# Optimization experiments

Measured on AMD Instinct MI355X. Metric: run time of the kernel, lower is better.

Reference implementation:

```python
import jax, jax.numpy as jnp
import numpy as np

B, S, D = 1024, 64, 768      # batch, patch_num, embed_dim
POOL, TOPK = 30, 4           # prompt pool size, top-k
SEQ = TOPK + S               # 68 = args.prompt_length + patch_num
CT = 64                      # compress_token
LN_EPS = 1e-5


def _l2_normalize(x, axis):
    ss = jnp.sum(x * x, axis=axis, keepdims=True)
    return x * jax.lax.rsqrt(jnp.maximum(ss, 1e-12))


def _layernorm(x, g, b):
    m = jnp.mean(x, axis=-1, keepdims=True)
    v = jnp.mean((x - m) ** 2, axis=-1, keepdims=True)
    return (x - m) * jax.lax.rsqrt(v + LN_EPS) * g + b


def setup_inputs() -> dict:
    key = jax.random.key(0)
    ks = jax.random.split(key, 8)
    def lin(k, din, dout):
        return (jax.random.normal(k, (din, dout), jnp.float32) / np.sqrt(din)).astype(jnp.float32)
    return {
        "x_embed": jax.random.normal(ks[0], (B, S, D), jnp.float32),
        "prompt": jax.random.uniform(ks[1], (POOL, D), jnp.float32, -5.0, 5.0),
        # mlp_1: Linear(SEQ->CT), LN(CT), Linear(CT->CT), LN(CT)
        "w1a": lin(ks[2], SEQ, CT), "b1a": jnp.zeros((CT,), jnp.float32),
        "g1a": jnp.ones((CT,), jnp.float32), "be1a": jnp.zeros((CT,), jnp.float32),
        "w1b": lin(ks[3], CT, CT), "b1b": jnp.zeros((CT,), jnp.float32),
        "g1b": jnp.ones((CT,), jnp.float32), "be1b": jnp.zeros((CT,), jnp.float32),
        # mlp_2: Linear(D->D), LN(D), Linear(D->D), LN(D)
        "w2a": lin(ks[4], D, D), "b2a": jnp.zeros((D,), jnp.float32),
        "g2a": jnp.ones((D,), jnp.float32), "be2a": jnp.zeros((D,), jnp.float32),
        "w2b": lin(ks[5], D, D), "b2b": jnp.zeros((D,), jnp.float32),
        "g2b": jnp.ones((D,), jnp.float32), "be2b": jnp.zeros((D,), jnp.float32),
    }


def _mixer(x, w1a, b1a, g1a, be1a, w1b, b1b, g1b, be1b,
           w2a, b2a, g2a, be2a, w2b, b2b, g2b, be2b):
    # x: (B, SEQ, D)
    x = jnp.swapaxes(x, 1, 2)                                   # (B, D, SEQ)
    x = _layernorm(jax.nn.relu(x @ w1a + b1a), g1a, be1a)       # (B, D, CT)
    x = _layernorm(jax.nn.relu(x @ w1b + b1b), g1b, be1b)
    x = jnp.swapaxes(x, 1, 2)                                   # (B, CT, D)
    x = _layernorm(jax.nn.relu(x @ w2a + b2a), g2a, be2a)
    x = _layernorm(jax.nn.relu(x @ w2b + b2b), g2b, be2b)
    return x


def reference(x_embed, prompt,
              w1a, b1a, g1a, be1a, w1b, b1b, g1b, be1b,
              w2a, b2a, g2a, be2a, w2b, b2b, g2b, be2b):
    # embedding key: mean over sequence
    x_mean = jnp.mean(x_embed, axis=1)                  # (B, D)
    prompt_norm = _l2_normalize(prompt, axis=1)         # (POOL, D)
    x_norm = _l2_normalize(x_mean, axis=1)              # (B, D)
    similarity = x_norm @ prompt_norm.T                 # (B, POOL)
    _, idx = jax.lax.top_k(similarity, TOPK)            # (B, TOPK), sorted desc
    batched_prompt = prompt[idx]                        # (B, TOPK, D)  (length=1 collapsed)
    selected_key = prompt_norm[idx]                     # (B, TOPK, D)
    reduce_sim = jnp.sum(selected_key * x_norm[:, None, :]) / x_embed.shape[0]
    x = jnp.concatenate([batched_prompt, x_embed], axis=1)  # (B, SEQ, D)
    prompted = _mixer(x, w1a, b1a, g1a, be1a, w1b, b1b, g1b, be1b,
                      w2a, b2a, g2a, be2a, w2b, b2b, g2b, be2b)  # (B, CT, D)
    return prompted, reduce_sim, similarity, idx
```

## Files before the change

### kernel.cpp

```cpp
#include <hip/hip_runtime.h>

#define B_    1024
#define S_    64
#define D_    768
#define POOL_ 30
#define TOPK_ 4
#define SEQ_  68
#define CT_   64

#define OUT_NP    50331648ull
#define OUT_RSIM  50331648ull
#define OUT_SIM   50331649ull
#define OUT_IDX   50362369ull

typedef short s16x8 __attribute__((ext_vector_type(8)));
typedef float f32x4 __attribute__((ext_vector_type(4)));
typedef unsigned short u16;

__device__ __forceinline__ u16 f2bf(float f){
  unsigned u = __float_as_uint(f);
  u += 0x7fff + ((u >> 16) & 1);
  return (u16)(u >> 16);
}

__global__ void prep_small(const float* __restrict__ prompt,
                           const float* __restrict__ w1a,
                           const float* __restrict__ w1b,
                           float* __restrict__ pnorm2,
                           u16* __restrict__ w1aT, u16* __restrict__ w1bT){
  int t = threadIdx.x;
  if (blockIdx.x == 0){
    if (t < 240){
      int j = t >> 3, seg = t & 7;
      float s = 0.f;
      for (int d = seg*96; d < seg*96 + 96; ++d){ float v = prompt[j*768 + d]; s += v*v; }
      #pragma unroll
      for (int m = 1; m < 8; m <<= 1) s += __shfl_xor(s, m);
      if (seg == 0) pnorm2[j] = rsqrtf(fmaxf(s, 1e-12f));
    }
  } else if (blockIdx.x == 1){
    for (int e = t; e < 6144; e += 256){
      int frag = e >> 3, el = e & 7;
      int lane = frag & 63, tile = frag >> 6;
      int nt = tile / 3, ks = tile % 3;
      int k  = ks*32 + (lane >> 4)*8 + el;
      int ct = nt*16 + (lane & 15);
      w1aT[e] = f2bf(k < SEQ_ ? w1a[k*64 + ct] : 0.f);
    }
  } else {
    for (int e = t; e < 4096; e += 256){
      int frag = e >> 3, el = e & 7;
      int lane = frag & 63, tile = frag >> 6;
      int nt = tile >> 1, ks = tile & 1;
      int k  = ks*32 + (lane >> 4)*8 + el;
      int n  = nt*16 + (lane & 15);
      w1bT[e] = f2bf(w1b[k*64 + n]);
    }
  }
}

__global__ void pack_w(const float* __restrict__ w2a,
                       const float* __restrict__ w2b,
                       u16* __restrict__ Wpka, u16* __restrict__ Wpkb){
  int lane = threadIdx.x;
  int ntg = blockIdx.x, ks = blockIdx.y;
  const float* w = blockIdx.z ? w2b : w2a;
  u16* wp = (blockIdx.z ? Wpkb : Wpka) + ((size_t)(ntg*24 + ks)*64 + lane)*8;
  int n  = ntg*16 + (lane & 15);
  int k0 = ks*32 + (lane >> 4)*8;
  #pragma unroll
  for (int e = 0; e < 8; ++e) wp[e] = f2bf(w[(size_t)(k0 + e)*768 + n]);
}

__global__ void sim_topk(const float* __restrict__ xe,
                         const float* __restrict__ prompt,
                         const float* __restrict__ pnorm2,
                         float* __restrict__ out, int* __restrict__ idx_int){
  __shared__ f32x4 ps[4][192];
  __shared__ f32x4 xm4s[192];
  __shared__ float wred[4];
  __shared__ float rsx_sh;
  __shared__ float simv[30];
  int b = blockIdx.x, t = threadIdx.x;
  int lane = t & 63, wv = t >> 6;

  const f32x4* xrow = (const f32x4*)(xe + (size_t)b*64*768);
  f32x4 a0 = {0.f,0.f,0.f,0.f}, a1 = a0, a2 = a0;
  #pragma unroll
  for (int r = 0; r < 16; ++r){
    const f32x4* rp = xrow + (size_t)(wv*16 + r)*192;
    a0 += rp[lane]; a1 += rp[lane + 64]; a2 += rp[lane + 128];
  }
  ps[wv][lane] = a0; ps[wv][lane + 64] = a1; ps[wv][lane + 128] = a2;
  __syncthreads();

  if (t < 192){
    f32x4 s = ps[0][t] + ps[1][t] + ps[2][t] + ps[3][t];
    s *= (1.f/64.f);
    xm4s[t] = s;
  }
  __syncthreads();

  if (wv == 0){
    f32x4 v0 = xm4s[lane], v1 = xm4s[lane + 64], v2 = xm4s[lane + 128];
    float n = v0[0]*v0[0]+v0[1]*v0[1]+v0[2]*v0[2]+v0[3]*v0[3]
            + v1[0]*v1[0]+v1[1]*v1[1]+v1[2]*v1[2]+v1[3]*v1[3]
            + v2[0]*v2[0]+v2[1]*v2[1]+v2[2]*v2[2]+v2[3]*v2[3];
    #pragma unroll
    for (int m = 1; m < 64; m <<= 1) n += __shfl_xor(n, m);
    if (lane == 0) rsx_sh = rsqrtf(fmaxf(n, 1e-12f));
  }
  __syncthreads();

  if (t < 240){
    int j = t >> 3, seg = t & 7;
    const f32x4* pj = (const f32x4*)(prompt + j*768) + seg*24;
    const f32x4* xm = xm4s + seg*24;
    float s = 0.f;
    #pragma unroll
    for (int i = 0; i < 24; ++i){
      f32x4 p = pj[i], x = xm[i];
      s += p[0]*x[0] + p[1]*x[1] + p[2]*x[2] + p[3]*x[3];
    }
    #pragma unroll
    for (int m = 1; m < 8; m <<= 1) s += __shfl_xor(s, m);
    if (seg == 0){
      float sim = s * rsx_sh * pnorm2[j];
      out[OUT_SIM + (size_t)b*30 + j] = sim;
      simv[j] = sim;
    }
  }
  __syncthreads();

  if (t == 0){
    float racc = 0.f;
    for (int k = 0; k < 4; ++k){
      float best = -1e30f; int bi = 0;
      for (int j = 0; j < 30; ++j){ float v = simv[j]; if (v > best){ best = v; bi = j; } }
      simv[bi] = -1e30f;
      idx_int[b*4 + k] = bi;
      out[OUT_IDX + (size_t)b*4 + k] = (float)bi;
      racc += best;
    }
    atomicAdd(&out[OUT_RSIM], racc * (1.f/1024.f));
  }
}

__global__ void stage1(const float* __restrict__ xe, const float* __restrict__ prompt,
                       const int* __restrict__ idx_int,
                       const u16* __restrict__ w1aT, const u16* __restrict__ w1bT,
                       const float* __restrict__ b1a, const float* __restrict__ g1a, const float* __restrict__ be1a,
                       const float* __restrict__ b1b, const float* __restrict__ g1b, const float* __restrict__ be1b,
                       u16* __restrict__ Tg){
  __shared__ __align__(16) unsigned char sm[43136];
  u16* As_pk      = (u16*)sm;
  u16 (*A2s)[72]  = (u16(*)[72])(sm + 24704);
  u16 (*Ts)[136]  = (u16(*)[136])sm;

  int t = threadIdx.x;
  int b = blockIdx.y, d0 = blockIdx.x * 128;

  #pragma unroll
  for (int p = 0; p < 12; ++p){
    int item = t + 512*p;
    int dd = item & 127, jp = item >> 7;
    int j = jp << 1;
    float v0 = 0.f, v1 = 0.f;
    if (j < 4){
      v0 = prompt[(size_t)idx_int[b*4 + j    ]*768 + d0 + dd];
      v1 = prompt[(size_t)idx_int[b*4 + j + 1]*768 + d0 + dd];
    } else if (j < 68){
      const float* xp = xe + ((size_t)b*64 + (j-4))*768 + d0 + dd;
      v0 = xp[0];
      v1 = xp[768];
    }
    unsigned pk = (unsigned)f2bf(v0) | ((unsigned)f2bf(v1) << 16);
    int idx16 = (dd>>4)*1544 + (j>>5)*512 + ((j>>3)&3)*128 + (dd&15)*8 + (j&7);
    *(unsigned*)&As_pk[idx16] = pk;
  }
  __syncthreads();

  int wv = t >> 6, lane = t & 63, quad = lane >> 4, l15 = lane & 15;
  int mrow = wv*16 + l15;

  f32x4 acc[4];
  #pragma unroll
  for (int nt = 0; nt < 4; ++nt) acc[nt] = (f32x4){0.f,0.f,0.f,0.f};
  #pragma unroll
  for (int ks = 0; ks < 3; ++ks){
    s16x8 a = *(const s16x8*)&As_pk[wv*1544 + ks*512 + lane*8];
    #pragma unroll
    for (int nt = 0; nt < 4; ++nt){
      s16x8 bf = *(const s16x8*)(w1aT + ((nt*3 + ks)*64 + lane)*8);
      acc[nt] = __builtin_amdgcn_mfma_f32_16x16x32_bf16(a, bf, acc[nt], 0, 0, 0);
    }
  }
  {
    float s1[4] = {0,0,0,0}, s2[4] = {0,0,0,0};
    #pragma unroll
    for (int nt = 0; nt < 4; ++nt){
      float bb = b1a[nt*16 + l15];
      #pragma unroll
      for (int i = 0; i < 4; ++i){
        float v = fmaxf(acc[nt][i] + bb, 0.f);
        acc[nt][i] = v; s1[i] += v; s2[i] += v*v;
      }
    }
    #pragma unroll
    for (int i = 0; i < 4; ++i){
      #pragma unroll
      for (int m = 1; m < 16; m <<= 1){ s1[i] += __shfl_xor(s1[i], m); s2[i] += __shfl_xor(s2[i], m); }
    }
    #pragma unroll
    for (int i = 0; i < 4; ++i){
      float mean = s1[i]*(1.f/64.f);
      float var  = s2[i]*(1.f/64.f) - mean*mean;
      float rs   = rsqrtf(var + 1e-5f);
      int row = wv*16 + quad*4 + i;
      #pragma unroll
      for (int nt = 0; nt < 4; ++nt){
        int ct = nt*16 + l15;
        A2s[row][ct] = f2bf((acc[nt][i] - mean)*rs*g1a[ct] + be1a[ct]);
      }
    }
  }
  __syncthreads();

  f32x4 acc2[4];
  #pragma unroll
  for (int nt = 0; nt < 4; ++nt) acc2[nt] = (f32x4){0.f,0.f,0.f,0.f};
  #pragma unroll
  for (int ks = 0; ks < 2; ++ks){
    s16x8 a = *(const s16x8*)&A2s[mrow][ks*32 + quad*8];
    #pragma unroll
    for (int nt = 0; nt < 4; ++nt){
      s16x8 bf = *(const s16x8*)(w1bT + ((nt*2 + ks)*64 + lane)*8);
      acc2[nt] = __builtin_amdgcn_mfma_f32_16x16x32_bf16(a, bf, acc2[nt], 0, 0, 0);
    }
  }
  {
    float s1[4] = {0,0,0,0}, s2[4] = {0,0,0,0};
    #pragma unroll
    for (int nt = 0; nt < 4; ++nt){
      float bb = b1b[nt*16 + l15];
      #pragma unroll
      for (int i = 0; i < 4; ++i){
        float v = fmaxf(acc2[nt][i] + bb, 0.f);
        acc2[nt][i] = v; s1[i] += v; s2[i] += v*v;
      }
    }
    #pragma unroll
    for (int i = 0; i < 4; ++i){
      #pragma unroll
      for (int m = 1; m < 16; m <<= 1){ s1[i] += __shfl_xor(s1[i], m); s2[i] += __shfl_xor(s2[i], m); }
    }
    #pragma unroll
    for (int i = 0; i < 4; ++i){
      float mean = s1[i]*(1.f/64.f);
      float var  = s2[i]*(1.f/64.f) - mean*mean;
      float rs   = rsqrtf(var + 1e-5f);
      int row = wv*16 + quad*4 + i;
      #pragma unroll
      for (int nt = 0; nt < 4; ++nt){
        int ct = nt*16 + l15;
        Ts[ct][row] = f2bf((acc2[nt][i] - mean)*rs*g1b[ct] + be1b[ct]);
      }
    }
  }
  __syncthreads();

  #pragma unroll
  for (int c = t; c < 1024; c += 512){
    int ct = c >> 4, off = (c & 15)*8;
    *(s16x8*)(Tg + ((size_t)(b*64 + ct))*768 + d0 + off) = *(const s16x8*)&Ts[ct][off];
  }
}

__device__ __forceinline__ void gemm_ln_768(
    const u16* __restrict__ Wpk, const float* __restrict__ bias,
    const float* __restrict__ g, const float* __restrict__ be,
    u16 (*Arows)[776], float (*red)[64][8], float (*redt)[64],
    float* __restrict__ outp, int row0, int t, bool final_store)
{
  int wv = t >> 6, lane = t & 63, quad = lane >> 4, l15 = lane & 15;
  f32x4 acc[4][6];
  #pragma unroll
  for (int mt = 0; mt < 4; ++mt)
    #pragma unroll
    for (int nt = 0; nt < 6; ++nt) acc[mt][nt] = (f32x4){0.f,0.f,0.f,0.f};

  const u16* wbase = Wpk + (size_t)wv*73728 + (size_t)lane*8;

  s16x8 bnxt[6];
  #pragma unroll
  for (int nt = 0; nt < 6; ++nt)
    bnxt[nt] = *(const s16x8*)(wbase + nt*12288);

  #pragma unroll
  for (int ks = 0; ks < 24; ++ks){
    s16x8 bcur[6];
    #pragma unroll
    for (int nt = 0; nt < 6; ++nt) bcur[nt] = bnxt[nt];
    if (ks < 23){
      #pragma unroll
      for (int nt = 0; nt < 6; ++nt)
        bnxt[nt] = *(const s16x8*)(wbase + nt*12288 + (ks+1)*512);
    }
    s16x8 a[4];
    #pragma unroll
    for (int mt = 0; mt < 4; ++mt)
      a[mt] = *(const s16x8*)&Arows[mt*16 + l15][ks*32 + quad*8];
    #pragma unroll
    for (int nt = 0; nt < 6; ++nt){
      #pragma unroll
      for (int mt = 0; mt < 4; ++mt)
        acc[mt][nt] = __builtin_amdgcn_mfma_f32_16x16x32_bf16(a[mt], bcur[nt], acc[mt][nt], 0, 0, 0);
    }
  }

  float s1[4][4], s2[4][4];
  #pragma unroll
  for (int mt = 0; mt < 4; ++mt)
    #pragma unroll
    for (int i = 0; i < 4; ++i){ s1[mt][i] = 0.f; s2[mt][i] = 0.f; }
  #pragma unroll
  for (int nt = 0; nt < 6; ++nt){
    float bb = bias[wv*96 + nt*16 + l15];
    #pragma unroll
    for (int mt = 0; mt < 4; ++mt){
      #pragma unroll
      for (int i = 0; i < 4; ++i){
        float v = fmaxf(acc[mt][nt][i] + bb, 0.f);
        acc[mt][nt][i] = v; s1[mt][i] += v; s2[mt][i] += v*v;
      }
    }
  }
  #pragma unroll
  for (int mt = 0; mt < 4; ++mt){
    #pragma unroll
    for (int i = 0; i < 4; ++i){
      #pragma unroll
      for (int m = 1; m < 16; m <<= 1){
        s1[mt][i] += __shfl_xor(s1[mt][i], m);
        s2[mt][i] += __shfl_xor(s2[mt][i], m);
      }
    }
  }
  if (l15 == 0){
    #pragma unroll
    for (int mt = 0; mt < 4; ++mt)
      #pragma unroll
      for (int i = 0; i < 4; ++i){
        int row = mt*16 + quad*4 + i;
        red[0][row][wv] = s1[mt][i]; red[1][row][wv] = s2[mt][i];
      }
  }
  __syncthreads();
  if (t < 128){
    int r = t >> 1, p = t & 1;
    float s = 0.f;
    #pragma unroll
    for (int w = 0; w < 8; ++w) s += red[p][r][w];
    redt[p][r] = s;
  }
  __syncthreads();
  #pragma unroll
  for (int mt = 0; mt < 4; ++mt){
    #pragma unroll
    for (int i = 0; i < 4; ++i){
      int row = mt*16 + quad*4 + i;
      float mean = redt[0][row]*(1.f/768.f);
      float var  = redt[1][row]*(1.f/768.f) - mean*mean;
      float rs   = rsqrtf(var + 1e-5f);
      #pragma unroll
      for (int nt = 0; nt < 6; ++nt){
        int col = wv*96 + nt*16 + l15;
        float v = (acc[mt][nt][i] - mean)*rs*g[col] + be[col];
        if (final_store) outp[(size_t)(row0 + row)*768 + col] = v;
        else             Arows[row][col] = f2bf(v);
      }
    }
  }
}

__global__ __launch_bounds__(512, 2)
void stage2(const u16* __restrict__ Tg,
            const u16* __restrict__ Wpka, const u16* __restrict__ Wpkb,
            const float* __restrict__ b2a, const float* __restrict__ g2a, const float* __restrict__ be2a,
            const float* __restrict__ b2b, const float* __restrict__ g2b, const float* __restrict__ be2b,
            float* __restrict__ out){
  __shared__ __align__(16) u16 Arows[64][776];
  __shared__ float red[2][64][8];
  __shared__ float redt[2][64];
  int t = threadIdx.x;
  int row0 = blockIdx.x * 64;
  #pragma unroll
  for (int c = t; c < 6144; c += 512){
    int r = c / 96, off = (c % 96)*8;
    *(s16x8*)&Arows[r][off] = *(const s16x8*)(Tg + (size_t)(row0 + r)*768 + off);
  }
  __syncthreads();
  gemm_ln_768(Wpka, b2a, g2a, be2a, Arows, red, redt, out, row0, t, false);
  __syncthreads();
  gemm_ln_768(Wpkb, b2b, g2b, be2b, Arows, red, redt, out, row0, t, true);
}

extern "C" void kernel_launch(void* const* d_in, const int* in_sizes, int n_in,
                              void* d_out, int out_size, void* d_ws, size_t ws_size,
                              hipStream_t stream){
  (void)in_sizes; (void)n_in; (void)out_size; (void)ws_size;
  const float* xe     = (const float*)d_in[0];
  const float* prompt = (const float*)d_in[1];
  const float* w1a = (const float*)d_in[2],  *b1a = (const float*)d_in[3];
  const float* g1a = (const float*)d_in[4],  *be1a= (const float*)d_in[5];
  const float* w1b = (const float*)d_in[6],  *b1b = (const float*)d_in[7];
  const float* g1b = (const float*)d_in[8],  *be1b= (const float*)d_in[9];
  const float* w2a = (const float*)d_in[10], *b2a = (const float*)d_in[11];
  const float* g2a = (const float*)d_in[12], *be2a= (const float*)d_in[13];
  const float* w2b = (const float*)d_in[14], *b2b = (const float*)d_in[15];
  const float* g2b = (const float*)d_in[16], *be2b= (const float*)d_in[17];
  float* out = (float*)d_out;

  char* ws = (char*)d_ws;
  u16*   Tg     = (u16*)(ws);
  u16*   Wpka   = (u16*)(ws + 100663296);
  u16*   Wpkb   = (u16*)(ws + 101842944);
  u16*   w1aT   = (u16*)(ws + 103022592);
  u16*   w1bT   = (u16*)(ws + 103034880);
  float* pnorm2 = (float*)(ws + 103043072);
  int*   idx_i  = (int*)(ws + 103043200);

  hipMemsetAsync((char*)d_out + OUT_RSIM*sizeof(float), 0, sizeof(float), stream);
  prep_small<<<3, 256, 0, stream>>>(prompt, w1a, w1b, pnorm2, w1aT, w1bT);
  pack_w<<<dim3(48,24,2), 64, 0, stream>>>(w2a, w2b, Wpka, Wpkb);
  sim_topk<<<B_, 256, 0, stream>>>(xe, prompt, pnorm2, out, idx_i);
  stage1<<<dim3(6, B_), 512, 0, stream>>>(xe, prompt, idx_i, w1aT, w1bT,
                                          b1a, g1a, be1a, b1b, g1b, be1b, Tg);
  stage2<<<1024, 512, 0, stream>>>(Tg, Wpka, Wpkb, b2a, g2a, be2a, b2b, g2b, be2b, out);
}
```

Before: 637.5 us.

## Fuse sim/topk, token-mixing and channel MLP into one per-batch kernel

```diff
diff --git a/kernel.cpp b/kernel.cpp
--- a/kernel.cpp
+++ b/kernel.cpp
@@ -21,6 +21,10 @@
   unsigned u = __float_as_uint(f);
   u += 0x7fff + ((u >> 16) & 1);
   return (u16)(u >> 16);
+}
+
+__device__ __forceinline__ int ar_idx(int row, int col){
+  return row*776 + (col & ~63) + ((((col >> 3) + row) & 7) << 3) + (col & 7);
 }
 
 __global__ void prep_small(const float* __restrict__ prompt,
@@ -72,217 +76,15 @@
   for (int e = 0; e < 8; ++e) wp[e] = f2bf(w[(size_t)(k0 + e)*768 + n]);
 }
 
-__global__ void sim_topk(const float* __restrict__ xe,
-                         const float* __restrict__ prompt,
-                         const float* __restrict__ pnorm2,
-                         float* __restrict__ out, int* __restrict__ idx_int){
-  __shared__ f32x4 ps[4][192];
-  __shared__ f32x4 xm4s[192];
-  __shared__ float wred[4];
-  __shared__ float rsx_sh;
-  __shared__ float simv[30];
-  int b = blockIdx.x, t = threadIdx.x;
-  int lane = t & 63, wv = t >> 6;
-
-  const f32x4* xrow = (const f32x4*)(xe + (size_t)b*64*768);
-  f32x4 a0 = {0.f,0.f,0.f,0.f}, a1 = a0, a2 = a0;
-  #pragma unroll
-  for (int r = 0; r < 16; ++r){
-    const f32x4* rp = xrow + (size_t)(wv*16 + r)*192;
-    a0 += rp[lane]; a1 += rp[lane + 64]; a2 += rp[lane + 128];
-  }
-  ps[wv][lane] = a0; ps[wv][lane + 64] = a1; ps[wv][lane + 128] = a2;
-  __syncthreads();
-
-  if (t < 192){
-    f32x4 s = ps[0][t] + ps[1][t] + ps[2][t] + ps[3][t];
-    s *= (1.f/64.f);
-    xm4s[t] = s;
-  }
-  __syncthreads();
-
-  if (wv == 0){
-    f32x4 v0 = xm4s[lane], v1 = xm4s[lane + 64], v2 = xm4s[lane + 128];
-    float n = v0[0]*v0[0]+v0[1]*v0[1]+v0[2]*v0[2]+v0[3]*v0[3]
-            + v1[0]*v1[0]+v1[1]*v1[1]+v1[2]*v1[2]+v1[3]*v1[3]
-            + v2[0]*v2[0]+v2[1]*v2[1]+v2[2]*v2[2]+v2[3]*v2[3];
-    #pragma unroll
-    for (int m = 1; m < 64; m <<= 1) n += __shfl_xor(n, m);
-    if (lane == 0) rsx_sh = rsqrtf(fmaxf(n, 1e-12f));
-  }
-  __syncthreads();
-
-  if (t < 240){
-    int j = t >> 3, seg = t & 7;
-    const f32x4* pj = (const f32x4*)(prompt + j*768) + seg*24;
-    const f32x4* xm = xm4s + seg*24;
-    float s = 0.f;
-    #pragma unroll
-    for (int i = 0; i < 24; ++i){
-      f32x4 p = pj[i], x = xm[i];
-      s += p[0]*x[0] + p[1]*x[1] + p[2]*x[2] + p[3]*x[3];
-    }
-    #pragma unroll
-    for (int m = 1; m < 8; m <<= 1) s += __shfl_xor(s, m);
-    if (seg == 0){
-      float sim = s * rsx_sh * pnorm2[j];
-      out[OUT_SIM + (size_t)b*30 + j] = sim;
-      simv[j] = sim;
-    }
-  }
-  __syncthreads();
-
-  if (t == 0){
-    float racc = 0.f;
-    for (int k = 0; k < 4; ++k){
-      float best = -1e30f; int bi = 0;
-      for (int j = 0; j < 30; ++j){ float v = simv[j]; if (v > best){ best = v; bi = j; } }
-      simv[bi] = -1e30f;
-      idx_int[b*4 + k] = bi;
-      out[OUT_IDX + (size_t)b*4 + k] = (float)bi;
-      racc += best;
-    }
-    atomicAdd(&out[OUT_RSIM], racc * (1.f/1024.f));
-  }
-}
-
-__global__ void stage1(const float* __restrict__ xe, const float* __restrict__ prompt,
-                       const int* __restrict__ idx_int,
-                       const u16* __restrict__ w1aT, const u16* __restrict__ w1bT,
-                       const float* __restrict__ b1a, const float* __restrict__ g1a, const float* __restrict__ be1a,
-                       const float* __restrict__ b1b, const float* __restrict__ g1b, const float* __restrict__ be1b,
-                       u16* __restrict__ Tg){
-  __shared__ __align__(16) unsigned char sm[43136];
-  u16* As_pk      = (u16*)sm;
-  u16 (*A2s)[72]  = (u16(*)[72])(sm + 24704);
-  u16 (*Ts)[136]  = (u16(*)[136])sm;
-
-  int t = threadIdx.x;
-  int b = blockIdx.y, d0 = blockIdx.x * 128;
-
-  #pragma unroll
-  for (int p = 0; p < 12; ++p){
-    int item = t + 512*p;
-    int dd = item & 127, jp = item >> 7;
-    int j = jp << 1;
-    float v0 = 0.f, v1 = 0.f;
-    if (j < 4){
-      v0 = prompt[(size_t)idx_int[b*4 + j    ]*768 + d0 + dd];
-      v1 = prompt[(size_t)idx_int[b*4 + j + 1]*768 + d0 + dd];
-    } else if (j < 68){
-      const float* xp = xe + ((size_t)b*64 + (j-4))*768 + d0 + dd;
-      v0 = xp[0];
-      v1 = xp[768];
-    }
-    unsigned pk = (unsigned)f2bf(v0) | ((unsigned)f2bf(v1) << 16);
-    int idx16 = (dd>>4)*1544 + (j>>5)*512 + ((j>>3)&3)*128 + (dd&15)*8 + (j&7);
-    *(unsigned*)&As_pk[idx16] = pk;
-  }
-  __syncthreads();
-
-  int wv = t >> 6, lane = t & 63, quad = lane >> 4, l15 = lane & 15;
-  int mrow = wv*16 + l15;
-
-  f32x4 acc[4];
-  #pragma unroll
-  for (int nt = 0; nt < 4; ++nt) acc[nt] = (f32x4){0.f,0.f,0.f,0.f};
-  #pragma unroll
-  for (int ks = 0; ks < 3; ++ks){
-    s16x8 a = *(const s16x8*)&As_pk[wv*1544 + ks*512 + lane*8];
-    #pragma unroll
-    for (int nt = 0; nt < 4; ++nt){
-      s16x8 bf = *(const s16x8*)(w1aT + ((nt*3 + ks)*64 + lane)*8);
-      acc[nt] = __builtin_amdgcn_mfma_f32_16x16x32_bf16(a, bf, acc[nt], 0, 0, 0);
-    }
-  }
-  {
-    float s1[4] = {0,0,0,0}, s2[4] = {0,0,0,0};
-    #pragma unroll
-    for (int nt = 0; nt < 4; ++nt){
-      float bb = b1a[nt*16 + l15];
-      #pragma unroll
-      for (int i = 0; i < 4; ++i){
-        float v = fmaxf(acc[nt][i] + bb, 0.f);
-        acc[nt][i] = v; s1[i] += v; s2[i] += v*v;
-      }
-    }
-    #pragma unroll
-    for (int i = 0; i < 4; ++i){
-      #pragma unroll
-      for (int m = 1; m < 16; m <<= 1){ s1[i] += __shfl_xor(s1[i], m); s2[i] += __shfl_xor(s2[i], m); }
-    }
-    #pragma unroll
-    for (int i = 0; i < 4; ++i){
-      float mean = s1[i]*(1.f/64.f);
-      float var  = s2[i]*(1.f/64.f) - mean*mean;
-      float rs   = rsqrtf(var + 1e-5f);
-      int row = wv*16 + quad*4 + i;
-      #pragma unroll
-      for (int nt = 0; nt < 4; ++nt){
-        int ct = nt*16 + l15;
-        A2s[row][ct] = f2bf((acc[nt][i] - mean)*rs*g1a[ct] + be1a[ct]);
-      }
-    }
-  }
-  __syncthreads();
-
-  f32x4 acc2[4];
-  #pragma unroll
-  for (int nt = 0; nt < 4; ++nt) acc2[nt] = (f32x4){0.f,0.f,0.f,0.f};
-  #pragma unroll
-  for (int ks = 0; ks < 2; ++ks){
-    s16x8 a = *(const s16x8*)&A2s[mrow][ks*32 + quad*8];
-    #pragma unroll
-    for (int nt = 0; nt < 4; ++nt){
-      s16x8 bf = *(const s16x8*)(w1bT + ((nt*2 + ks)*64 + lane)*8);
-      acc2[nt] = __builtin_amdgcn_mfma_f32_16x16x32_bf16(a, bf, acc2[nt], 0, 0, 0);
-    }
-  }
-  {
-    float s1[4] = {0,0,0,0}, s2[4] = {0,0,0,0};
-    #pragma unroll
-    for (int nt = 0; nt < 4; ++nt){
-      float bb = b1b[nt*16 + l15];
-      #pragma unroll
-      for (int i = 0; i < 4; ++i){
-        float v = fmaxf(acc2[nt][i] + bb, 0.f);
-        acc2[nt][i] = v; s1[i] += v; s2[i] += v*v;
-      }
-    }
-    #pragma unroll
-    for (int i = 0; i < 4; ++i){
-      #pragma unroll
-      for (int m = 1; m < 16; m <<= 1){ s1[i] += __shfl_xor(s1[i], m); s2[i] += __shfl_xor(s2[i], m); }
-    }
-    #pragma unroll
-    for (int i = 0; i < 4; ++i){
-      float mean = s1[i]*(1.f/64.f);
-      float var  = s2[i]*(1.f/64.f) - mean*mean;
-      float rs   = rsqrtf(var + 1e-5f);
-      int row = wv*16 + quad*4 + i;
-      #pragma unroll
-      for (int nt = 0; nt < 4; ++nt){
-        int ct = nt*16 + l15;
-        Ts[ct][row] = f2bf((acc2[nt][i] - mean)*rs*g1b[ct] + be1b[ct]);
-      }
-    }
-  }
-  __syncthreads();
-
-  #pragma unroll
-  for (int c = t; c < 1024; c += 512){
-    int ct = c >> 4, off = (c & 15)*8;
-    *(s16x8*)(Tg + ((size_t)(b*64 + ct))*768 + d0 + off) = *(const s16x8*)&Ts[ct][off];
-  }
-}
-
+template<bool FINAL>
 __device__ __forceinline__ void gemm_ln_768(
     const u16* __restrict__ Wpk, const float* __restrict__ bias,
     const float* __restrict__ g, const float* __restrict__ be,
-    u16 (*Arows)[776], float (*red)[64][8], float (*redt)[64],
-    float* __restrict__ outp, int row0, int t, bool final_store)
+    u16* __restrict__ Arows, float (*red)[64][8], float (*redt)[64],
+    float* __restrict__ outp, int row0, int t)
 {
   int wv = t >> 6, lane = t & 63, quad = lane >> 4, l15 = lane & 15;
+  int h = l15 & 7;
   f32x4 acc[4][6];
   #pragma unroll
   for (int mt = 0; mt < 4; ++mt)
@@ -291,32 +93,46 @@
 
   const u16* wbase = Wpk + (size_t)wv*73728 + (size_t)lane*8;
 
-  s16x8 bnxt[6];
-  #pragma unroll
-  for (int nt = 0; nt < 6; ++nt)
-    bnxt[nt] = *(const s16x8*)(wbase + nt*12288);
-
-  #pragma unroll
-  for (int ks = 0; ks < 24; ++ks){
-    s16x8 bcur[6];
-    #pragma unroll
-    for (int nt = 0; nt < 6; ++nt) bcur[nt] = bnxt[nt];
-    if (ks < 23){
-      #pragma unroll
-      for (int nt = 0; nt < 6; ++nt)
-        bnxt[nt] = *(const s16x8*)(wbase + nt*12288 + (ks+1)*512);
-    }
-    s16x8 a[4];
-    #pragma unroll
-    for (int mt = 0; mt < 4; ++mt)
-      a[mt] = *(const s16x8*)&Arows[mt*16 + l15][ks*32 + quad*8];
-    #pragma unroll
-    for (int nt = 0; nt < 6; ++nt){
-      #pragma unroll
-      for (int mt = 0; mt < 4; ++mt)
-        acc[mt][nt] = __builtin_amdgcn_mfma_f32_16x16x32_bf16(a[mt], bcur[nt], acc[mt][nt], 0, 0, 0);
-    }
-  }
+  const u16* Ap0[4]; const u16* Ap1[4];
+  #pragma unroll
+  for (int mt = 0; mt < 4; ++mt){
+    int rb = (mt*16 + l15)*776;
+    Ap0[mt] = Arows + rb + (((quad     + h) & 7) << 3);
+    Ap1[mt] = Arows + rb + (((quad + 4 + h) & 7) << 3);
+  }
+
+  s16x8 bX[6], bY[6], bZ[6];
+  #pragma unroll
+  for (int nt = 0; nt < 6; ++nt) bX[nt] = *(const s16x8*)(wbase + nt*12288);
+  #pragma unroll
+  for (int nt = 0; nt < 6; ++nt) bY[nt] = *(const s16x8*)(wbase + nt*12288 + 512);
+
+#define GSTEP(CUR, PRE, KS)                                                    \
+  {                                                                            \
+    if ((KS)+2 < 24){                                                          \
+      _Pragma("unroll")                                                        \
+      for (int nt = 0; nt < 6; ++nt)                                           \
+        PRE[nt] = *(const s16x8*)(wbase + nt*12288 + ((KS)+2)*512);            \
+    }                                                                          \
+    s16x8 a_[4];                                                               \
+    _Pragma("unroll")                                                          \
+    for (int mt = 0; mt < 4; ++mt)                                             \
+      a_[mt] = *(const s16x8*)(( ((KS)&1) ? Ap1[mt] : Ap0[mt] ) + ((KS)>>1)*64);\
+    _Pragma("unroll")                                                          \
+    for (int nt = 0; nt < 6; ++nt){                                            \
+      _Pragma("unroll")                                                        \
+      for (int mt = 0; mt < 4; ++mt)                                           \
+        acc[mt][nt] = __builtin_amdgcn_mfma_f32_16x16x32_bf16(a_[mt], CUR[nt], acc[mt][nt], 0, 0, 0); \
+    }                                                                          \
+  }
+
+  #pragma unroll
+  for (int kp = 0; kp < 8; ++kp){
+    GSTEP(bX, bZ, kp*3+0)
+    GSTEP(bY, bX, kp*3+1)
+    GSTEP(bZ, bY, kp*3+2)
+  }
+#undef GSTEP
 
   float s1[4][4], s2[4][4];
   #pragma unroll
@@ -376,33 +192,219 @@
       for (int nt = 0; nt < 6; ++nt){
         int col = wv*96 + nt*16 + l15;
         float v = (acc[mt][nt][i] - mean)*rs*g[col] + be[col];
-        if (final_store) outp[(size_t)(row0 + row)*768 + col] = v;
-        else             Arows[row][col] = f2bf(v);
+        if (FINAL) outp[(size_t)(row0 + row)*768 + col] = v;
+        else       Arows[ar_idx(row, col)] = f2bf(v);
       }
     }
   }
 }
 
 __global__ __launch_bounds__(512, 2)
-void stage2(const u16* __restrict__ Tg,
-            const u16* __restrict__ Wpka, const u16* __restrict__ Wpkb,
-            const float* __restrict__ b2a, const float* __restrict__ g2a, const float* __restrict__ be2a,
-            const float* __restrict__ b2b, const float* __restrict__ g2b, const float* __restrict__ be2b,
-            float* __restrict__ out){
-  __shared__ __align__(16) u16 Arows[64][776];
+void fused(const float* __restrict__ xe, const float* __restrict__ prompt,
+           const float* __restrict__ pnorm2,
+           const u16* __restrict__ w1aT, const u16* __restrict__ w1bT,
+           const float* __restrict__ b1a, const float* __restrict__ g1a, const float* __restrict__ be1a,
+           const float* __restrict__ b1b, const float* __restrict__ g1b, const float* __restrict__ be1b,
+           const u16* __restrict__ Wpka, const u16* __restrict__ Wpkb,
+           const float* __restrict__ b2a, const float* __restrict__ g2a, const float* __restrict__ be2a,
+           const float* __restrict__ b2b, const float* __restrict__ g2b, const float* __restrict__ be2b,
+           float* __restrict__ out)
+{
+  __shared__ __align__(16) u16 Arows[64*776];
+  __shared__ __align__(16) unsigned char scr[43136];
   __shared__ float red[2][64][8];
   __shared__ float redt[2][64];
-  int t = threadIdx.x;
-  int row0 = blockIdx.x * 64;
-  #pragma unroll
-  for (int c = t; c < 6144; c += 512){
-    int r = c / 96, off = (c % 96)*8;
-    *(s16x8*)&Arows[r][off] = *(const s16x8*)(Tg + (size_t)(row0 + r)*768 + off);
-  }
+  __shared__ float simv[30];
+  __shared__ float rsx_sh;
+  __shared__ int   idxs[4];
+
+  int b = blockIdx.x, t = threadIdx.x;
+  int lane = t & 63, wv = t >> 6, quad = lane >> 4, l15 = lane & 15;
+
+  {
+    f32x4 (*ps)[192] = (f32x4(*)[192])scr;
+    f32x4* xm4s = (f32x4*)(scr + 24576);
+    const f32x4* xrow = (const f32x4*)(xe + (size_t)b*49152);
+    f32x4 a0 = {0.f,0.f,0.f,0.f}, a1 = a0, a2 = a0;
+    #pragma unroll
+    for (int r = 0; r < 8; ++r){
+      const f32x4* rp = xrow + (size_t)(wv*8 + r)*192;
+      a0 += rp[lane]; a1 += rp[lane + 64]; a2 += rp[lane + 128];
+    }
+    ps[wv][lane] = a0; ps[wv][lane + 64] = a1; ps[wv][lane + 128] = a2;
+    __syncthreads();
+    if (t < 192){
+      f32x4 s = ps[0][t];
+      #pragma unroll
+      for (int w = 1; w < 8; ++w) s += ps[w][t];
+      s *= (1.f/64.f);
+      xm4s[t] = s;
+    }
+    __syncthreads();
+    if (wv == 0){
+      f32x4 v0 = xm4s[lane], v1 = xm4s[lane + 64], v2 = xm4s[lane + 128];
+      float n = v0[0]*v0[0]+v0[1]*v0[1]+v0[2]*v0[2]+v0[3]*v0[3]
+              + v1[0]*v1[0]+v1[1]*v1[1]+v1[2]*v1[2]+v1[3]*v1[3]
+              + v2[0]*v2[0]+v2[1]*v2[1]+v2[2]*v2[2]+v2[3]*v2[3];
+      #pragma unroll
+      for (int m = 1; m < 64; m <<= 1) n += __shfl_xor(n, m);
+      if (lane == 0) rsx_sh = rsqrtf(fmaxf(n, 1e-12f));
+    }
+    __syncthreads();
+    if (t < 240){
+      int j = t >> 3, seg = t & 7;
+      const f32x4* pj = (const f32x4*)(prompt + j*768) + seg*24;
+      const f32x4* xm = xm4s + seg*24;
+      float s = 0.f;
+      #pragma unroll
+      for (int i = 0; i < 24; ++i){
+        f32x4 p = pj[i], x = xm[i];
+        s += p[0]*x[0] + p[1]*x[1] + p[2]*x[2] + p[3]*x[3];
+      }
+      #pragma unroll
+      for (int m = 1; m < 8; m <<= 1) s += __shfl_xor(s, m);
+      if (seg == 0){
+        float sim = s * rsx_sh * pnorm2[j];
+        out[OUT_SIM + (size_t)b*30 + j] = sim;
+        simv[j] = sim;
+      }
+    }
+    __syncthreads();
+    if (t == 0){
+      float racc = 0.f;
+      for (int k = 0; k < 4; ++k){
+        float best = -1e30f; int bi = 0;
+        for (int j = 0; j < 30; ++j){ float v = simv[j]; if (v > best){ best = v; bi = j; } }
+        simv[bi] = -1e30f;
+        idxs[k] = bi;
+        out[OUT_IDX + (size_t)b*4 + k] = (float)bi;
+        racc += best;
+      }
+      atomicAdd(&out[OUT_RSIM], racc * (1.f/1024.f));
+    }
+    __syncthreads();
+  }
+
+  {
+    u16* As_pk     = (u16*)scr;
+    u16 (*A2s)[72] = (u16(*)[72])(scr + 24704);
+
+    s16x8 wa[12], wb[8];
+    #pragma unroll
+    for (int f = 0; f < 12; ++f) wa[f] = *(const s16x8*)(w1aT + (f*64 + lane)*8);
+    #pragma unroll
+    for (int f = 0; f < 8; ++f)  wb[f] = *(const s16x8*)(w1bT + (f*64 + lane)*8);
+
+    int mrow = wv*16 + l15;
+    for (int c6 = 0; c6 < 6; ++c6){
+      int d0 = c6*128;
+      #pragma unroll
+      for (int p = 0; p < 12; ++p){
+        int item = t + 512*p;
+        int dd = item & 127, jp = item >> 7;
+        int j = jp << 1;
+        float v0 = 0.f, v1 = 0.f;
+        if (j < 4){
+          v0 = prompt[(size_t)idxs[j    ]*768 + d0 + dd];
+          v1 = prompt[(size_t)idxs[j + 1]*768 + d0 + dd];
+        } else if (j < 68){
+          const float* xp = xe + ((size_t)b*64 + (j-4))*768 + d0 + dd;
+          v0 = xp[0];
+          v1 = xp[768];
+        }
+        unsigned pk = (unsigned)f2bf(v0) | ((unsigned)f2bf(v1) << 16);
+        int idx16 = (dd>>4)*1544 + (j>>5)*512 + ((j>>3)&3)*128 + (dd&15)*8 + (j&7);
+        *(unsigned*)&As_pk[idx16] = pk;
+      }
+      __syncthreads();
+
+      f32x4 acc[4];
+      #pragma unroll
+      for (int nt = 0; nt < 4; ++nt) acc[nt] = (f32x4){0.f,0.f,0.f,0.f};
+      #pragma unroll
+      for (int ks = 0; ks < 3; ++ks){
+        s16x8 a = *(const s16x8*)&As_pk[wv*1544 + ks*512 + lane*8];
+        #pragma unroll
+        for (int nt = 0; nt < 4; ++nt)
+          acc[nt] = __builtin_amdgcn_mfma_f32_16x16x32_bf16(a, wa[nt*3 + ks], acc[nt], 0, 0, 0);
+      }
+      {
+        float s1[4] = {0,0,0,0}, s2[4] = {0,0,0,0};
+        #pragma unroll
+        for (int nt = 0; nt < 4; ++nt){
+          float bb = b1a[nt*16 + l15];
+          #pragma unroll
+          for (int i = 0; i < 4; ++i){
+            float v = fmaxf(acc[nt][i] + bb, 0.f);
+            acc[nt][i] = v; s1[i] += v; s2[i] += v*v;
+          }
+        }
+        #pragma unroll
+        for (int i = 0; i < 4; ++i){
+          #pragma unroll
+          for (int m = 1; m < 16; m <<= 1){ s1[i] += __shfl_xor(s1[i], m); s2[i] += __shfl_xor(s2[i], m); }
+        }
+        #pragma unroll
+        for (int i = 0; i < 4; ++i){
+          float mean = s1[i]*(1.f/64.f);
+          float var  = s2[i]*(1.f/64.f) - mean*mean;
+          float rs   = rsqrtf(var + 1e-5f);
+          int row = wv*16 + quad*4 + i;
+          #pragma unroll
+          for (int nt = 0; nt < 4; ++nt){
+            int ct = nt*16 + l15;
+            A2s[row][ct] = f2bf((acc[nt][i] - mean)*rs*g1a[ct] + be1a[ct]);
+          }
+        }
+      }
+      __syncthreads();
+
+      f32x4 acc2[4];
+      #pragma unroll
+      for (int nt = 0; nt < 4; ++nt) acc2[nt] = (f32x4){0.f,0.f,0.f,0.f};
+      #pragma unroll
+      for (int ks = 0; ks < 2; ++ks){
+        s16x8 a = *(const s16x8*)&A2s[mrow][ks*32 + quad*8];
+        #pragma unroll
+        for (int nt = 0; nt < 4; ++nt)
+          acc2[nt] = __builtin_amdgcn_mfma_f32_16x16x32_bf16(a, wb[nt*2 + ks], acc2[nt], 0, 0, 0);
+      }
+      {
+        float s1[4] = {0,0,0,0}, s2[4] = {0,0,0,0};
+        #pragma unroll
+        for (int nt = 0; nt < 4; ++nt){
+          float bb = b1b[nt*16 + l15];
+          #pragma unroll
+          for (int i = 0; i < 4; ++i){
+            float v = fmaxf(acc2[nt][i] + bb, 0.f);
+            acc2[nt][i] = v; s1[i] += v; s2[i] += v*v;
+          }
+        }
+        #pragma unroll
+        for (int i = 0; i < 4; ++i){
+          #pragma unroll
+          for (int m = 1; m < 16; m <<= 1){ s1[i] += __shfl_xor(s1[i], m); s2[i] += __shfl_xor(s2[i], m); }
+        }
+        #pragma unroll
+        for (int i = 0; i < 4; ++i){
+          float mean = s1[i]*(1.f/64.f);
+          float var  = s2[i]*(1.f/64.f) - mean*mean;
+          float rs   = rsqrtf(var + 1e-5f);
+          int drow = wv*16 + quad*4 + i;
+          #pragma unroll
+          for (int nt = 0; nt < 4; ++nt){
+            int ct = nt*16 + l15;
+            Arows[ar_idx(ct, d0 + drow)] = f2bf((acc2[nt][i] - mean)*rs*g1b[ct] + be1b[ct]);
+          }
+        }
+      }
+      __syncthreads();
+    }
+  }
+
+  gemm_ln_768<false>(Wpka, b2a, g2a, be2a, Arows, red, redt, out, b*64, t);
   __syncthreads();
-  gemm_ln_768(Wpka, b2a, g2a, be2a, Arows, red, redt, out, row0, t, false);
-  __syncthreads();
-  gemm_ln_768(Wpkb, b2b, g2b, be2b, Arows, red, redt, out, row0, t, true);
+  gemm_ln_768<true >(Wpkb, b2b, g2b, be2b, Arows, red, redt, out, b*64, t);
 }
 
 extern "C" void kernel_launch(void* const* d_in, const int* in_sizes, int n_in,
@@ -422,19 +424,17 @@
   float* out = (float*)d_out;
 
   char* ws = (char*)d_ws;
-  u16*   Tg     = (u16*)(ws);
-  u16*   Wpka   = (u16*)(ws + 100663296);
-  u16*   Wpkb   = (u16*)(ws + 101842944);
-  u16*   w1aT   = (u16*)(ws + 103022592);
-  u16*   w1bT   = (u16*)(ws + 103034880);
-  float* pnorm2 = (float*)(ws + 103043072);
-  int*   idx_i  = (int*)(ws + 103043200);
+  u16*   Wpka   = (u16*)(ws);
+  u16*   Wpkb   = (u16*)(ws + 1179648);
+  u16*   w1aT   = (u16*)(ws + 2359296);
+  u16*   w1bT   = (u16*)(ws + 2371584);
+  float* pnorm2 = (float*)(ws + 2379776);
 
   hipMemsetAsync((char*)d_out + OUT_RSIM*sizeof(float), 0, sizeof(float), stream);
   prep_small<<<3, 256, 0, stream>>>(prompt, w1a, w1b, pnorm2, w1aT, w1bT);
   pack_w<<<dim3(48,24,2), 64, 0, stream>>>(w2a, w2b, Wpka, Wpkb);
-  sim_topk<<<B_, 256, 0, stream>>>(xe, prompt, pnorm2, out, idx_i);
-  stage1<<<dim3(6, B_), 512, 0, stream>>>(xe, prompt, idx_i, w1aT, w1bT,
-                                          b1a, g1a, be1a, b1b, g1b, be1b, Tg);
-  stage2<<<1024, 512, 0, stream>>>(Tg, Wpka, Wpkb, b2a, g2a, be2a, b2b, g2b, be2b, out);
-}
+  fused<<<B_, 512, 0, stream>>>(xe, prompt, pnorm2, w1aT, w1bT,
+                                b1a, g1a, be1a, b1b, g1b, be1b,
+                                Wpka, Wpkb,
+                                b2a, g2a, be2a, b2b, g2b, be2b, out);
+}
```

After: 666.9 us. 1.05x slower.
